# Kernel optimization log

Hardware: AMD Instinct MI355X
Metric: run time of the kernel (lower is better)

The kernel has to match this reference:

```python
import jax, jax.numpy as jnp
import numpy as np

SCAD_A = 3.7
PERCENTILE_Q = 0.75
EPS = 1e-8
LAM_HAT = 0.9
PROP_STEP = 4


def setup_inputs() -> dict:
    key = jax.random.key(0)
    ks = jax.random.split(key, 4)
    N, IN, H, OUT = 4096, 512, 256, 64
    p = 32.0 / N  # avg degree ~32 (pre-symmetrization ~64 after OR, still sparse)
    u = jax.random.uniform(ks[0], (N, N))
    Au = u < p
    Asym = Au | Au.T
    eye = jnp.eye(N, dtype=bool)
    A = jnp.where(eye, 0.0, Asym.astype(jnp.float32))  # zero diagonal; add_loops adds I
    X = jax.random.normal(ks[1], (N, IN), dtype=jnp.float32)
    W1 = jax.random.normal(ks[2], (IN, H), dtype=jnp.float32) / np.sqrt(IN)
    b1 = jnp.zeros((H,), dtype=jnp.float32)
    W2 = jax.random.normal(ks[3], (H, OUT), dtype=jnp.float32) / np.sqrt(H)
    b2 = jnp.zeros((OUT,), dtype=jnp.float32)
    log_gamma_0 = jnp.asarray(np.log(3.0), dtype=jnp.float32)
    raw_decay = jnp.asarray(np.log(0.85 / 0.15), dtype=jnp.float32)
    raw_alpha_blend = jnp.asarray(0.0, dtype=jnp.float32)  # sigmoid -> 0.5 blend
    return {"A": A, "X": X, "W1": W1, "b1": b1, "W2": W2, "b2": b2,
            "log_gamma_0": log_gamma_0, "raw_decay": raw_decay,
            "raw_alpha_blend": raw_alpha_blend}


def _scad_weight(y, lam, a):
    # SCAD-derived reweighting: 1 for y<=lam, (a*lam - y)/((a-1)*y) in the middle, 0 beyond a*lam.
    y_safe = jnp.maximum(y, EPS)  # avoid inf/nan in unselected branch (forward value unchanged)
    w_mid = (a * lam - y) / ((a - 1.0) * y_safe)
    return jnp.where(y <= lam, 1.0, jnp.where(y <= a * lam, w_mid, 0.0))


def reference(A, X, W1, b1, W2, b2, log_gamma_0, raw_decay, raw_alpha_blend):
    N = A.shape[0]
    eye = jnp.eye(N, dtype=A.dtype)
    Ahat = A + eye                          # add_loops
    D = Ahat.sum(-1)                        # [N]
    D_sq = jnp.sqrt(D)[:, None]             # [N,1]
    A_tilde = Ahat / (D_sq * D_sq.T)        # sym_norm: D^{-1/2} A D^{-1/2}
    edge_mask = (Ahat > 0) & (eye == 0)     # A_bool & ~I
    has_edges = edge_mask.sum() > 0

    # MLP (eval mode: dropout inactive)
    F0 = jnp.maximum(X @ W1 + b1, 0.0) @ W2 + b2   # [N, out_dim]

    alpha = jax.nn.sigmoid(raw_alpha_blend)
    g0 = jnp.exp(log_gamma_0)
    r = jax.nn.sigmoid(raw_decay)
    lam = 1.0 / LAM_HAT - 1.0

    Fc = F0
    for k in range(PROP_STEP):
        gamma_param_k = g0 * (r ** k)
        Fn = Fc / D_sq
        nrm = jnp.linalg.norm(Fn, axis=-1, keepdims=True)
        Fu = Fn / jnp.maximum(nrm, EPS)     # F.normalize semantics
        y = jnp.clip(1.0 - Fu @ Fu.T, 0.0, 2.0)  # [N,N] cosine distance
        y = jax.lax.stop_gradient(y)        # y.detach()
        y_edges = jnp.where(edge_mask, y, jnp.nan)
        gamma_data_k = jnp.nanquantile(y_edges, PERCENTILE_Q)
        gamma_data_k = jnp.maximum(jnp.where(has_edges, gamma_data_k, 1.0), EPS)
        lam_combined = alpha * (gamma_param_k / SCAD_A) + (1.0 - alpha) * (gamma_data_k / SCAD_A)
        W = _scad_weight(y, lam_combined, SCAD_A)
        W = W * (1.0 - eye)
        W = jnp.where(jnp.isnan(W), 1.0, W)
        Q_hat = ((W * Ahat).sum(-1) / D + lam)[:, None]
        Fc = (W * A_tilde) @ Fc / Q_hat + lam * F0 / Q_hat
    return Fc
```

## Files before the change

kernel.cpp:

```cpp
#include <hip/hip_runtime.h>
#include <math.h>

#define N_NODES 4096
#define IN_DIM  512
#define H_DIM   256
#define OUT_DIM 64
#define SCAD_Af 3.7f
#define EPSf    1e-8f
#define NBINS   8192
#define MAXD    256
#define KSPLIT  4

__device__ __forceinline__ float scad_w(float y, float lamc) {
    if (y <= lamc) return 1.0f;
    if (y <= SCAD_Af * lamc)
        return (SCAD_Af * lamc - y) / ((SCAD_Af - 1.0f) * fmaxf(y, EPSf));
    return 0.0f;
}

__global__ __launch_bounds__(256)
void k_init(const float* __restrict__ A, const float* __restrict__ X,
            const float* __restrict__ W1, float* __restrict__ part,
            int* __restrict__ colIdx, int* __restrict__ rowcnt,
            float* __restrict__ D, float* __restrict__ isD,
            unsigned int* __restrict__ hist01) {
    __shared__ float As[16][68];
    __shared__ float Bs[16][64];
    __shared__ int cnt4[4];
    int tid = threadIdx.x;
    if (blockIdx.x < 1024) {
        int blk = blockIdx.x;
        int bx = blk & 3, by = (blk >> 2) & 63, bz = blk >> 8;
        int tx = tid & 15, ty = tid >> 4;
        int bm = by * 64, bn = bx * 64;
        int kbeg = bz * (IN_DIM / KSPLIT);
        float acc[4][4] = {};
        for (int k0 = kbeg; k0 < kbeg + IN_DIM / KSPLIT; k0 += 16) {
            {
                int r = tid >> 2, kv = tid & 3;
                float4 v = *(const float4*)(X + (size_t)(bm + r) * IN_DIM + k0 + kv * 4);
                As[kv * 4 + 0][r] = v.x;
                As[kv * 4 + 1][r] = v.y;
                As[kv * 4 + 2][r] = v.z;
                As[kv * 4 + 3][r] = v.w;
            }
            {
                int kk = tid >> 4, nv = tid & 15;
                *(float4*)&Bs[kk][nv * 4] =
                    *(const float4*)(W1 + (size_t)(k0 + kk) * H_DIM + bn + nv * 4);
            }
            __syncthreads();
#pragma unroll
            for (int kk = 0; kk < 16; kk++) {
                float a[4], b[4];
#pragma unroll
                for (int u = 0; u < 4; u++) { a[u] = As[kk][ty * 4 + u]; b[u] = Bs[kk][tx * 4 + u]; }
#pragma unroll
                for (int u = 0; u < 4; u++)
#pragma unroll
                    for (int v = 0; v < 4; v++) acc[u][v] += a[u] * b[v];
            }
            __syncthreads();
        }
        float* Cm = part + (size_t)bz * N_NODES * H_DIM;
#pragma unroll
        for (int u = 0; u < 4; u++) {
            int m = bm + ty * 4 + u;
#pragma unroll
            for (int v = 0; v < 4; v++)
                Cm[(size_t)m * H_DIM + bn + tx * 4 + v] = acc[u][v];
        }
    } else {
        int bb = blockIdx.x - 1024;
        int gid2 = bb * 256 + tid;
        if (gid2 < 2 * NBINS) hist01[gid2] = 0u;
        int w = tid >> 6, lane = tid & 63;
        int i = bb * 4 + w;
        if (lane == 0) cnt4[w] = 0;
        __syncthreads();
        const float4* row4 = (const float4*)(A + (size_t)i * N_NODES);
        int* ci = colIdx + i * MAXD;
        for (int v = lane; v < N_NODES / 4; v += 64) {
            float4 x = row4[v];
            int j0 = v * 4;
            if (x.x != 0.0f) { int p = atomicAdd(&cnt4[w], 1); ci[p] = j0; }
            if (x.y != 0.0f) { int p = atomicAdd(&cnt4[w], 1); ci[p] = j0 + 1; }
            if (x.z != 0.0f) { int p = atomicAdd(&cnt4[w], 1); ci[p] = j0 + 2; }
            if (x.w != 0.0f) { int p = atomicAdd(&cnt4[w], 1); ci[p] = j0 + 3; }
        }
        __syncthreads();
        if (lane == 0) {
            int t = cnt4[w];
            rowcnt[i] = t;
            float d = (float)t + 1.0f;
            D[i] = d;
            isD[i] = 1.0f / sqrtf(d);
        }
    }
}

__global__ __launch_bounds__(256)
void k_mlp2(const float* __restrict__ part, const float* __restrict__ b1,
            const float* __restrict__ W2, const float* __restrict__ b2,
            const int* __restrict__ rowcnt, const float* __restrict__ isD,
            float* __restrict__ F0, float* __restrict__ Fu, int* __restrict__ nE) {
    __shared__ float sh_h[4][H_DIM];
    int tid = threadIdx.x;
    if (blockIdx.x == 0) {
        __shared__ unsigned int ps[256];
        unsigned int s = 0;
        for (int q = tid; q < N_NODES; q += 256) s += (unsigned int)rowcnt[q];
        ps[tid] = s;
        __syncthreads();
        for (int off = 128; off; off >>= 1) {
            if (tid < off) ps[tid] += ps[tid + off];
            __syncthreads();
        }
        if (tid == 0) nE[0] = (int)ps[0];
    }
    int w = tid >> 6, lane = tid & 63;
    int i = blockIdx.x * 4 + w;
    const size_t tot = (size_t)N_NODES * H_DIM;
    const float* p0 = part + (size_t)i * H_DIM;
#pragma unroll
    for (int q = 0; q < 4; q++) {
        int k = q * 64 + lane;
        float s = p0[k] + p0[tot + k] + p0[2 * tot + k] + p0[3 * tot + k] + b1[k];
        sh_h[w][k] = fmaxf(s, 0.0f);
    }
    const float* W2c = W2 + lane;
    float a0 = 0, a1 = 0, a2 = 0, a3 = 0;
#pragma unroll 8
    for (int k = 0; k < H_DIM; k += 4) {
        a0 += sh_h[w][k + 0] * W2c[(k + 0) * OUT_DIM];
        a1 += sh_h[w][k + 1] * W2c[(k + 1) * OUT_DIM];
        a2 += sh_h[w][k + 2] * W2c[(k + 2) * OUT_DIM];
        a3 += sh_h[w][k + 3] * W2c[(k + 3) * OUT_DIM];
    }
    float f0 = (a0 + a1) + (a2 + a3) + b2[lane];
    F0[(size_t)i * 64 + lane] = f0;
    float fn = f0 * isD[i];
    float s2 = fn * fn;
    for (int off = 32; off; off >>= 1) s2 += __shfl_xor(s2, off, 64);
    Fu[(size_t)i * 64 + lane] = fn / fmaxf(sqrtf(s2), EPSf);
}

__global__ __launch_bounds__(256)
void k_edgehist(const float* __restrict__ Fu, const int* __restrict__ rowcnt,
                const int* __restrict__ colIdx, float* __restrict__ y_e,
                unsigned int* __restrict__ histK) {
    __shared__ unsigned int hl[NBINS];
    for (int b = threadIdx.x; b < NBINS; b += 256) hl[b] = 0u;
    __syncthreads();
    int gid = blockIdx.x * 256 + threadIdx.x;
    int ri = gid >> 6;
    int lane = threadIdx.x & 63;
    int eg = lane >> 2, el = lane & 3;
    int deg = rowcnt[ri];
    const float4* Fu4 = (const float4*)Fu;
    float4 fi0 = Fu4[ri * 16 + el * 4 + 0];
    float4 fi1 = Fu4[ri * 16 + el * 4 + 1];
    float4 fi2 = Fu4[ri * 16 + el * 4 + 2];
    float4 fi3 = Fu4[ri * 16 + el * 4 + 3];
    for (int base = 0; base < deg; base += 16) {
        int e = base + eg;
        bool act = e < deg;
        int j = act ? colIdx[ri * MAXD + e] : ri;
        float4 a0 = Fu4[(size_t)j * 16 + el * 4 + 0];
        float4 a1 = Fu4[(size_t)j * 16 + el * 4 + 1];
        float4 a2 = Fu4[(size_t)j * 16 + el * 4 + 2];
        float4 a3 = Fu4[(size_t)j * 16 + el * 4 + 3];
        float s = fi0.x * a0.x + fi0.y * a0.y + fi0.z * a0.z + fi0.w * a0.w
                + fi1.x * a1.x + fi1.y * a1.y + fi1.z * a1.z + fi1.w * a1.w
                + fi2.x * a2.x + fi2.y * a2.y + fi2.z * a2.z + fi2.w * a2.w
                + fi3.x * a3.x + fi3.y * a3.y + fi3.z * a3.z + fi3.w * a3.w;
        s += __shfl_xor(s, 1, 64);
        s += __shfl_xor(s, 2, 64);
        if (act && el == 0) {
            float y = 1.0f - s;
            y = fminf(fmaxf(y, 0.0f), 2.0f);
            y_e[ri * MAXD + e] = y;
            int bin = (int)(y * (NBINS * 0.5f));
            if (bin > NBINS - 1) bin = NBINS - 1;
            atomicAdd(&hl[bin], 1u);
        }
    }
    __syncthreads();
    for (int b = threadIdx.x; b < NBINS; b += 256) {
        unsigned int v = hl[b];
        if (v) atomicAdd(&histK[b], v);
    }
}

__global__ __launch_bounds__(256)
void k_propq(const unsigned int* __restrict__ histK, unsigned int* __restrict__ histNext,
             const int* __restrict__ nEp, const int* __restrict__ rowcnt,
             const int* __restrict__ colIdx, const float* __restrict__ y_e,
             const float* __restrict__ Fc, const float* __restrict__ F0,
             const float* __restrict__ D, const float* __restrict__ isD,
             const float* __restrict__ lg0, const float* __restrict__ rdec,
             const float* __restrict__ ralpha, int kiter,
             float* __restrict__ Fout, float* __restrict__ FuNext) {
    __shared__ unsigned int psum[256];
    __shared__ float vv[2];
    __shared__ float sh_scal;
    int tid = threadIdx.x;
    int gid = blockIdx.x * 256 + tid;
    if (gid < NBINS) histNext[gid] = 0u;
    {
        unsigned int cnt[32];
        const uint4* h4 = (const uint4*)histK;
        unsigned int s = 0;
#pragma unroll
        for (int q = 0; q < 8; q++) {
            uint4 v = h4[tid * 8 + q];
            cnt[q * 4 + 0] = v.x; cnt[q * 4 + 1] = v.y;
            cnt[q * 4 + 2] = v.z; cnt[q * 4 + 3] = v.w;
            s += v.x + v.y + v.z + v.w;
        }
        psum[tid] = s;
        __syncthreads();
        for (int off = 1; off < 256; off <<= 1) {
            unsigned int x = 0;
            if (tid >= off) x = psum[tid - off];
            __syncthreads();
            psum[tid] += x;
            __syncthreads();
        }
        int nE = nEp[0];
        double h = 0.75 * (double)(nE - 1);
        long long i0 = (long long)h;
        float frac = (float)(h - (double)i0);
        unsigned int r0 = (unsigned int)i0, r1 = (unsigned int)(i0 + 1);
        unsigned int cum = (tid == 0) ? 0u : psum[tid - 1];
#pragma unroll
        for (int b = 0; b < 32; b++) {
            unsigned int cn = cnt[b];
            unsigned int lo = cum;
            cum += cn;
            if (cn) {
                float v = ((float)(tid * 32 + b) + 0.5f) * (2.0f / (float)NBINS);
                if (lo <= r0 && r0 < cum) vv[0] = v;
                if (lo <= r1 && r1 < cum) vv[1] = v;
            }
        }
        __syncthreads();
        if (tid == 0) {
            float gd = vv[0] + frac * (vv[1] - vv[0]);
            gd = fmaxf(gd, EPSf);
            float alpha = 1.0f / (1.0f + expf(-ralpha[0]));
            float g0 = expf(lg0[0]);
            float r = 1.0f / (1.0f + expf(-rdec[0]));
            float gp = g0;
            for (int q = 0; q < kiter; q++) gp *= r;
            sh_scal = alpha * (gp / SCAD_Af) + (1.0f - alpha) * (gd / SCAD_Af);
        }
        __syncthreads();
    }
    float lamc = sh_scal;
    const float lam = (float)(1.0 / 0.9 - 1.0);
    int i = gid >> 6, c = gid & 63;
    int deg = rowcnt[i];
    float acc = 0.0f, wsum = 0.0f;
    for (int base = 0; base < deg; base += 64) {
        int m = deg - base; if (m > 64) m = 64;
        int   jl = (c < m) ? colIdx[i * MAXD + base + c] : 0;
        float yl = (c < m) ? y_e[i * MAXD + base + c] : 9.0f;
        float il = (c < m) ? isD[jl] : 0.0f;
        int tt = 0;
        for (; tt + 4 <= m; tt += 4) {
            int j0 = __shfl(jl, tt, 64),     j1 = __shfl(jl, tt + 1, 64);
            int j2 = __shfl(jl, tt + 2, 64), j3 = __shfl(jl, tt + 3, 64);
            float f0 = Fc[(size_t)j0 * 64 + c], f1 = Fc[(size_t)j1 * 64 + c];
            float f2 = Fc[(size_t)j2 * 64 + c], f3 = Fc[(size_t)j3 * 64 + c];
            float s0 = scad_w(__shfl(yl, tt, 64),     lamc);
            float s1 = scad_w(__shfl(yl, tt + 1, 64), lamc);
            float s2 = scad_w(__shfl(yl, tt + 2, 64), lamc);
            float s3 = scad_w(__shfl(yl, tt + 3, 64), lamc);
            wsum += s0 + s1 + s2 + s3;
            acc += s0 * __shfl(il, tt, 64) * f0 + s1 * __shfl(il, tt + 1, 64) * f1
                 + s2 * __shfl(il, tt + 2, 64) * f2 + s3 * __shfl(il, tt + 3, 64) * f3;
        }
        for (; tt < m; tt++) {
            int   j = __shfl(jl, tt, 64);
            float y = __shfl(yl, tt, 64);
            float wq = scad_w(y, lamc);
            wsum += wq;
            acc += wq * __shfl(il, tt, 64) * Fc[(size_t)j * 64 + c];
        }
    }
    float Q = wsum / D[i] + lam;
    float fo = (isD[i] * acc + lam * F0[(size_t)i * 64 + c]) / Q;
    Fout[(size_t)i * 64 + c] = fo;
    float fn = fo * isD[i];
    float s2n = fn * fn;
    for (int off = 32; off; off >>= 1) s2n += __shfl_xor(s2n, off, 64);
    FuNext[(size_t)i * 64 + c] = fn / fmaxf(sqrtf(s2n), EPSf);
}

extern "C" void kernel_launch(void* const* d_in, const int* in_sizes, int n_in,
                              void* d_out, int out_size, void* d_ws, size_t ws_size,
                              hipStream_t stream) {
    const float* A      = (const float*)d_in[0];
    const float* X      = (const float*)d_in[1];
    const float* W1     = (const float*)d_in[2];
    const float* b1     = (const float*)d_in[3];
    const float* W2     = (const float*)d_in[4];
    const float* b2     = (const float*)d_in[5];
    const float* lg0    = (const float*)d_in[6];
    const float* rdec   = (const float*)d_in[7];
    const float* ralpha = (const float*)d_in[8];
    float* outp = (float*)d_out;

    char* w = (char*)d_ws;
    size_t off = 0;
    auto carve = [&](size_t bytes) -> char* {
        char* p = w + off;
        off += (bytes + 255) & ~(size_t)255;
        return p;
    };
    int*      colIdx = (int*)carve((size_t)N_NODES * MAXD * 4);
    float*    y_e    = (float*)carve((size_t)N_NODES * MAXD * 4);
    float*    part   = (float*)carve((size_t)KSPLIT * N_NODES * H_DIM * 4);
    int*      rowcnt = (int*)carve(N_NODES * 4);
    float*    D      = (float*)carve(N_NODES * 4);
    float*    isD    = (float*)carve(N_NODES * 4);
    float*    Fu     = (float*)carve((size_t)N_NODES * 64 * 4);
    float*    F0     = (float*)carve((size_t)N_NODES * 64 * 4);
    float*    FcA    = (float*)carve((size_t)N_NODES * 64 * 4);
    float*    FcB    = (float*)carve((size_t)N_NODES * 64 * 4);
    unsigned* hist01 = (unsigned*)carve(2 * NBINS * 4);
    int*      nE     = (int*)carve(256);

    k_init<<<dim3(2048), dim3(256), 0, stream>>>(A, X, W1, part, colIdx, rowcnt, D, isD, hist01);
    k_mlp2<<<dim3(1024), dim3(256), 0, stream>>>(part, b1, W2, b2, rowcnt, isD, F0, Fu, nE);

    const float* fin = F0;
    float* fouts[4] = {FcA, FcB, FcA, outp};
    for (int k = 0; k < 4; k++) {
        unsigned* histK    = hist01 + (k & 1) * NBINS;
        unsigned* histNext = hist01 + ((k + 1) & 1) * NBINS;
        k_edgehist<<<dim3(1024), dim3(256), 0, stream>>>(Fu, rowcnt, colIdx, y_e, histK);
        k_propq<<<dim3(1024), dim3(256), 0, stream>>>(histK, histNext, nE, rowcnt, colIdx,
                                                      y_e, fin, F0, D, isD, lg0, rdec,
                                                      ralpha, k, fouts[k], Fu);
        fin = fouts[k];
    }
}
```

Before: 342.8 us.

## Fuse all stages into one cooperative persistent kernel with grid syncs

Replaces the chain of ten kernel launches (init, MLP tail, and four edge-histogram/propagation pairs) with a single cooperative kernel of 1024 blocks that uses grid-wide syncs between phases. The A-row scan and the first GEMM now share one block pass, and the histogram is accumulated per block in shared memory before being flushed to global memory. The histogram bin count is also cut from 8192 to 2048, which coarsens the quantile estimate. The kernel falls back to the old multi-launch path if cooperative launch is unavailable or occupancy is too low. Grid syncs replace launch overhead but can stall the whole device, and folding both work halves into one block lengthens each block's work.

```diff
diff --git a/kernel.cpp b/kernel.cpp
--- a/kernel.cpp
+++ b/kernel.cpp
@@ -1,5 +1,8 @@
 #include <hip/hip_runtime.h>
+#include <hip/hip_cooperative_groups.h>
 #include <math.h>
+
+namespace cg = cooperative_groups;
 
 #define N_NODES 4096
 #define IN_DIM  512
@@ -7,7 +10,7 @@
 #define OUT_DIM 64
 #define SCAD_Af 3.7f
 #define EPSf    1e-8f
-#define NBINS   8192
+#define NBINS   2048
 #define MAXD    256
 #define KSPLIT  4
 
@@ -16,6 +19,288 @@
     if (y <= SCAD_Af * lamc)
         return (SCAD_Af * lamc - y) / ((SCAD_Af - 1.0f) * fmaxf(y, EPSf));
     return 0.0f;
+}
+
+__global__ __launch_bounds__(256, 4)
+void k_mega(const float* __restrict__ A,  const float* __restrict__ X,
+            const float* __restrict__ W1, const float* __restrict__ b1,
+            const float* __restrict__ W2, const float* __restrict__ b2,
+            const float* __restrict__ lg0, const float* __restrict__ rdec,
+            const float* __restrict__ ralpha,
+            int* __restrict__ colIdx, int* __restrict__ rowcnt,
+            float* __restrict__ D, float* __restrict__ isD,
+            float* __restrict__ Fu, float* __restrict__ part,
+            float* __restrict__ F0, float* __restrict__ FcA,
+            float* __restrict__ FcB, float* __restrict__ outp,
+            unsigned int* __restrict__ hist01, float* __restrict__ y_e) {
+    cg::grid_group grid = cg::this_grid();
+    const int tid = threadIdx.x;
+    const int blk = blockIdx.x;
+    const int gid = blk * 256 + tid;
+    const int w = tid >> 6, lane = tid & 63;
+
+    __shared__ union {
+        struct { float As[16][68]; float Bs[16][64]; } g;
+        unsigned int hl[NBINS];
+        unsigned int psum[256];
+        float sh_h[4][H_DIM];
+    } sm;
+    __shared__ float vv[2];
+    __shared__ float sh_scal;
+    __shared__ int   sh_nE;
+    __shared__ int   cnt4[4];
+
+    {
+        int i = blk * 4 + w;
+        if (lane == 0) cnt4[w] = 0;
+        __syncthreads();
+        const float4* row4 = (const float4*)(A + (size_t)i * N_NODES);
+        int* ci = colIdx + i * MAXD;
+        for (int v = lane; v < N_NODES / 4; v += 64) {
+            float4 x = row4[v];
+            int j0 = v * 4;
+            if (x.x != 0.0f) { int p = atomicAdd(&cnt4[w], 1); ci[p] = j0; }
+            if (x.y != 0.0f) { int p = atomicAdd(&cnt4[w], 1); ci[p] = j0 + 1; }
+            if (x.z != 0.0f) { int p = atomicAdd(&cnt4[w], 1); ci[p] = j0 + 2; }
+            if (x.w != 0.0f) { int p = atomicAdd(&cnt4[w], 1); ci[p] = j0 + 3; }
+        }
+        __syncthreads();
+        if (lane == 0) {
+            int t = cnt4[w];
+            rowcnt[i] = t;
+            float d = (float)t + 1.0f;
+            D[i] = d;
+            isD[i] = 1.0f / sqrtf(d);
+        }
+        if (gid < 2 * NBINS) hist01[gid] = 0u;
+        __syncthreads();
+    }
+    {
+        int bx = blk & 3, by = (blk >> 2) & 63, bz = blk >> 8;
+        int tx = tid & 15, ty = tid >> 4;
+        int bm = by * 64, bn = bx * 64;
+        int kbeg = bz * (IN_DIM / KSPLIT);
+        float acc[4][4] = {};
+        for (int k0 = kbeg; k0 < kbeg + IN_DIM / KSPLIT; k0 += 16) {
+            {
+                int r = tid >> 2, kv = tid & 3;
+                float4 v = *(const float4*)(X + (size_t)(bm + r) * IN_DIM + k0 + kv * 4);
+                sm.g.As[kv * 4 + 0][r] = v.x;
+                sm.g.As[kv * 4 + 1][r] = v.y;
+                sm.g.As[kv * 4 + 2][r] = v.z;
+                sm.g.As[kv * 4 + 3][r] = v.w;
+            }
+            {
+                int kk = tid >> 4, nv = tid & 15;
+                *(float4*)&sm.g.Bs[kk][nv * 4] =
+                    *(const float4*)(W1 + (size_t)(k0 + kk) * H_DIM + bn + nv * 4);
+            }
+            __syncthreads();
+#pragma unroll
+            for (int kk = 0; kk < 16; kk++) {
+                float a[4], b[4];
+#pragma unroll
+                for (int u = 0; u < 4; u++) { a[u] = sm.g.As[kk][ty * 4 + u]; b[u] = sm.g.Bs[kk][tx * 4 + u]; }
+#pragma unroll
+                for (int u = 0; u < 4; u++)
+#pragma unroll
+                    for (int v = 0; v < 4; v++) acc[u][v] += a[u] * b[v];
+            }
+            __syncthreads();
+        }
+        float* Cm = part + (size_t)bz * N_NODES * H_DIM;
+#pragma unroll
+        for (int u = 0; u < 4; u++) {
+            int m = bm + ty * 4 + u;
+#pragma unroll
+            for (int v = 0; v < 4; v++)
+                Cm[(size_t)m * H_DIM + bn + tx * 4 + v] = acc[u][v];
+        }
+    }
+    grid.sync();
+
+    {
+        unsigned int s = 0;
+        for (int q = tid; q < N_NODES; q += 256) s += (unsigned int)rowcnt[q];
+        sm.psum[tid] = s;
+        __syncthreads();
+        for (int off = 128; off; off >>= 1) {
+            if (tid < off) sm.psum[tid] += sm.psum[tid + off];
+            __syncthreads();
+        }
+        if (tid == 0) sh_nE = (int)sm.psum[0];
+        __syncthreads();
+
+        int i = blk * 4 + w;
+        const size_t tot = (size_t)N_NODES * H_DIM;
+        const float* p0 = part + (size_t)i * H_DIM;
+#pragma unroll
+        for (int q = 0; q < 4; q++) {
+            int k = q * 64 + lane;
+            float s2 = p0[k] + p0[tot + k] + p0[2 * tot + k] + p0[3 * tot + k] + b1[k];
+            sm.sh_h[w][k] = fmaxf(s2, 0.0f);
+        }
+        const float* W2c = W2 + lane;
+        float a0 = 0, a1 = 0, a2 = 0, a3 = 0;
+#pragma unroll 8
+        for (int k = 0; k < H_DIM; k += 4) {
+            a0 += sm.sh_h[w][k + 0] * W2c[(k + 0) * OUT_DIM];
+            a1 += sm.sh_h[w][k + 1] * W2c[(k + 1) * OUT_DIM];
+            a2 += sm.sh_h[w][k + 2] * W2c[(k + 2) * OUT_DIM];
+            a3 += sm.sh_h[w][k + 3] * W2c[(k + 3) * OUT_DIM];
+        }
+        float f0 = (a0 + a1) + (a2 + a3) + b2[lane];
+        F0[(size_t)i * 64 + lane] = f0;
+        float fn = f0 * isD[i];
+        float s2 = fn * fn;
+        for (int off = 32; off; off >>= 1) s2 += __shfl_xor(s2, off, 64);
+        Fu[(size_t)i * 64 + lane] = fn / fmaxf(sqrtf(s2), EPSf);
+    }
+    grid.sync();
+
+    const float lam = (float)(1.0 / 0.9 - 1.0);
+    const int eg = lane >> 2, el = lane & 3;
+    const int i = gid >> 6, c = gid & 63;
+    const float* fin = F0;
+    for (int k = 0; k < 4; k++) {
+        float* fout = (k == 0) ? FcA : (k == 1) ? FcB : (k == 2) ? FcA : outp;
+        unsigned int* histK    = hist01 + (k & 1) * NBINS;
+        unsigned int* histNext = hist01 + ((k + 1) & 1) * NBINS;
+
+        for (int b = tid; b < NBINS; b += 256) sm.hl[b] = 0u;
+        __syncthreads();
+        {
+            int ri = blk * 4 + w;
+            int deg = rowcnt[ri];
+            const float4* Fu4 = (const float4*)Fu;
+            float4 fi0 = Fu4[ri * 16 + el * 4 + 0];
+            float4 fi1 = Fu4[ri * 16 + el * 4 + 1];
+            float4 fi2 = Fu4[ri * 16 + el * 4 + 2];
+            float4 fi3 = Fu4[ri * 16 + el * 4 + 3];
+            for (int base = 0; base < deg; base += 16) {
+                int e = base + eg;
+                bool act = e < deg;
+                int j = act ? colIdx[ri * MAXD + e] : ri;
+                float4 a0 = Fu4[(size_t)j * 16 + el * 4 + 0];
+                float4 a1 = Fu4[(size_t)j * 16 + el * 4 + 1];
+                float4 a2 = Fu4[(size_t)j * 16 + el * 4 + 2];
+                float4 a3 = Fu4[(size_t)j * 16 + el * 4 + 3];
+                float s = fi0.x * a0.x + fi0.y * a0.y + fi0.z * a0.z + fi0.w * a0.w
+                        + fi1.x * a1.x + fi1.y * a1.y + fi1.z * a1.z + fi1.w * a1.w
+                        + fi2.x * a2.x + fi2.y * a2.y + fi2.z * a2.z + fi2.w * a2.w
+                        + fi3.x * a3.x + fi3.y * a3.y + fi3.z * a3.z + fi3.w * a3.w;
+                s += __shfl_xor(s, 1, 64);
+                s += __shfl_xor(s, 2, 64);
+                if (act && el == 0) {
+                    float y = 1.0f - s;
+                    y = fminf(fmaxf(y, 0.0f), 2.0f);
+                    y_e[ri * MAXD + e] = y;
+                    int bin = (int)(y * (NBINS * 0.5f));
+                    if (bin > NBINS - 1) bin = NBINS - 1;
+                    atomicAdd(&sm.hl[bin], 1u);
+                }
+            }
+        }
+        __syncthreads();
+        for (int b = tid; b < NBINS; b += 256) {
+            unsigned int v = sm.hl[b];
+            if (v) atomicAdd(&histK[b], v);
+        }
+        if (gid < NBINS) histNext[gid] = 0u;
+        grid.sync();
+
+        {
+            unsigned int cnt[8];
+            const uint4* h4 = (const uint4*)histK;
+            unsigned int s = 0;
+#pragma unroll
+            for (int q = 0; q < 2; q++) {
+                uint4 v = h4[tid * 2 + q];
+                cnt[q * 4 + 0] = v.x; cnt[q * 4 + 1] = v.y;
+                cnt[q * 4 + 2] = v.z; cnt[q * 4 + 3] = v.w;
+                s += v.x + v.y + v.z + v.w;
+            }
+            sm.psum[tid] = s;
+            __syncthreads();
+            for (int off = 1; off < 256; off <<= 1) {
+                unsigned int x = 0;
+                if (tid >= off) x = sm.psum[tid - off];
+                __syncthreads();
+                sm.psum[tid] += x;
+                __syncthreads();
+            }
+            int nE = sh_nE;
+            double h = 0.75 * (double)(nE - 1);
+            long long i0 = (long long)h;
+            float frac = (float)(h - (double)i0);
+            unsigned int r0 = (unsigned int)i0, r1 = (unsigned int)(i0 + 1);
+            unsigned int cum = (tid == 0) ? 0u : sm.psum[tid - 1];
+#pragma unroll
+            for (int b = 0; b < 8; b++) {
+                unsigned int cn = cnt[b];
+                unsigned int lo = cum;
+                cum += cn;
+                if (cn) {
+                    float v = ((float)(tid * 8 + b) + 0.5f) * (2.0f / (float)NBINS);
+                    if (lo <= r0 && r0 < cum) vv[0] = v;
+                    if (lo <= r1 && r1 < cum) vv[1] = v;
+                }
+            }
+            __syncthreads();
+            if (tid == 0) {
+                float gd = vv[0] + frac * (vv[1] - vv[0]);
+                gd = fmaxf(gd, EPSf);
+                float alpha = 1.0f / (1.0f + expf(-ralpha[0]));
+                float g0 = expf(lg0[0]);
+                float r = 1.0f / (1.0f + expf(-rdec[0]));
+                float gp = g0;
+                for (int q = 0; q < k; q++) gp *= r;
+                sh_scal = alpha * (gp / SCAD_Af) + (1.0f - alpha) * (gd / SCAD_Af);
+            }
+            __syncthreads();
+        }
+        {
+            float lamc = sh_scal;
+            int deg = rowcnt[i];
+            float acc = 0.0f, wsum = 0.0f;
+            for (int base = 0; base < deg; base += 64) {
+                int m = deg - base; if (m > 64) m = 64;
+                int   jl = (c < m) ? colIdx[i * MAXD + base + c] : 0;
+                float yl = (c < m) ? y_e[i * MAXD + base + c] : 9.0f;
+                float il = (c < m) ? isD[jl] : 0.0f;
+                int tt = 0;
+                for (; tt + 4 <= m; tt += 4) {
+                    int j0 = __shfl(jl, tt, 64),     j1 = __shfl(jl, tt + 1, 64);
+                    int j2 = __shfl(jl, tt + 2, 64), j3 = __shfl(jl, tt + 3, 64);
+                    float f0 = fin[(size_t)j0 * 64 + c], f1 = fin[(size_t)j1 * 64 + c];
+                    float f2 = fin[(size_t)j2 * 64 + c], f3 = fin[(size_t)j3 * 64 + c];
+                    float s0 = scad_w(__shfl(yl, tt, 64),     lamc);
+                    float s1 = scad_w(__shfl(yl, tt + 1, 64), lamc);
+                    float s2 = scad_w(__shfl(yl, tt + 2, 64), lamc);
+                    float s3 = scad_w(__shfl(yl, tt + 3, 64), lamc);
+                    wsum += s0 + s1 + s2 + s3;
+                    acc += s0 * __shfl(il, tt, 64) * f0 + s1 * __shfl(il, tt + 1, 64) * f1
+                         + s2 * __shfl(il, tt + 2, 64) * f2 + s3 * __shfl(il, tt + 3, 64) * f3;
+                }
+                for (; tt < m; tt++) {
+                    int   j = __shfl(jl, tt, 64);
+                    float y = __shfl(yl, tt, 64);
+                    float wq = scad_w(y, lamc);
+                    wsum += wq;
+                    acc += wq * __shfl(il, tt, 64) * fin[(size_t)j * 64 + c];
+                }
+            }
+            float Q = wsum / D[i] + lam;
+            float fo = (isD[i] * acc + lam * F0[(size_t)i * 64 + c]) / Q;
+            fout[(size_t)i * 64 + c] = fo;
+            float fn = fo * isD[i];
+            float s2n = fn * fn;
+            for (int off = 32; off; off >>= 1) s2n += __shfl_xor(s2n, off, 64);
+            Fu[(size_t)i * 64 + c] = fn / fmaxf(sqrtf(s2n), EPSf);
+        }
+        grid.sync();
+        fin = fout;
+    }
 }
 
 __global__ __launch_bounds__(256)
@@ -208,12 +493,12 @@
     int gid = blockIdx.x * 256 + tid;
     if (gid < NBINS) histNext[gid] = 0u;
     {
-        unsigned int cnt[32];
+        unsigned int cnt[8];
         const uint4* h4 = (const uint4*)histK;
         unsigned int s = 0;
 #pragma unroll
-        for (int q = 0; q < 8; q++) {
-            uint4 v = h4[tid * 8 + q];
+        for (int q = 0; q < 2; q++) {
+            uint4 v = h4[tid * 2 + q];
             cnt[q * 4 + 0] = v.x; cnt[q * 4 + 1] = v.y;
             cnt[q * 4 + 2] = v.z; cnt[q * 4 + 3] = v.w;
             s += v.x + v.y + v.z + v.w;
@@ -234,12 +519,12 @@
         unsigned int r0 = (unsigned int)i0, r1 = (unsigned int)(i0 + 1);
         unsigned int cum = (tid == 0) ? 0u : psum[tid - 1];
 #pragma unroll
-        for (int b = 0; b < 32; b++) {
+        for (int b = 0; b < 8; b++) {
             unsigned int cn = cnt[b];
             unsigned int lo = cum;
             cum += cn;
             if (cn) {
-                float v = ((float)(tid * 32 + b) + 0.5f) * (2.0f / (float)NBINS);
+                float v = ((float)(tid * 8 + b) + 0.5f) * (2.0f / (float)NBINS);
                 if (lo <= r0 && r0 < cum) vv[0] = v;
                 if (lo <= r1 && r1 < cum) vv[1] = v;
             }
@@ -332,9 +617,28 @@
     unsigned* hist01 = (unsigned*)carve(2 * NBINS * 4);
     int*      nE     = (int*)carve(256);
 
+    int coopAttr = 0, numCU = 0, maxPerCU = 0;
+    (void)hipDeviceGetAttribute(&coopAttr, hipDeviceAttributeCooperativeLaunch, 0);
+    (void)hipDeviceGetAttribute(&numCU, hipDeviceAttributeMultiprocessorCount, 0);
+    (void)hipOccupancyMaxActiveBlocksPerMultiprocessor(&maxPerCU, k_mega, 256, 0);
+    bool useCoop = (coopAttr != 0) && ((long)maxPerCU * (long)numCU >= 1024);
+
+    if (useCoop) {
+        void* args[] = {
+            (void*)&A, (void*)&X, (void*)&W1, (void*)&b1, (void*)&W2, (void*)&b2,
+            (void*)&lg0, (void*)&rdec, (void*)&ralpha,
+            (void*)&colIdx, (void*)&rowcnt, (void*)&D, (void*)&isD,
+            (void*)&Fu, (void*)&part, (void*)&F0,
+            (void*)&FcA, (void*)&FcB, (void*)&outp, (void*)&hist01, (void*)&y_e,
+        };
+        hipError_t e = hipLaunchCooperativeKernel((void*)k_mega, dim3(1024), dim3(256),
+                                                  args, 0, stream);
+        if (e == hipSuccess) return;
+        (void)hipGetLastError();
+    }
+
     k_init<<<dim3(2048), dim3(256), 0, stream>>>(A, X, W1, part, colIdx, rowcnt, D, isD, hist01);
     k_mlp2<<<dim3(1024), dim3(256), 0, stream>>>(part, b1, W2, b2, rowcnt, isD, F0, Fu, nE);
-
     const float* fin = F0;
     float* fouts[4] = {FcA, FcB, FcA, outp};
     for (int k = 0; k < 4; k++) {
```

Result: faster. 315.0 us (-8.1%).
